# Optimization experiments

Hardware: AMD Instinct MI355X
Metric: run time of the kernel (lower is better)

## Reference

```python
import jax, jax.numpy as jnp
import numpy as np

B, T = 64, 4096
H, I, F = 256, 7, 5
# MLP pyramid: in=H+F=261 -> 2^8..2^3 -> itera_dim
DIMS = [H + F, 256, 128, 64, 32, 16, 8, I]


def _uniform(key, shape, fan_in):
    s = 1.0 / np.sqrt(fan_in)
    return jax.random.uniform(key, shape, jnp.float32, -s, s)


def setup_inputs() -> dict:
    key = jax.random.key(0)
    ks = jax.random.split(key, 32)
    inp = {"x": jax.random.normal(ks[0], (B, T, I + F), jnp.float32)}
    # RNN params (torch nn.RNN layout: W_ih [H,I], W_hh [H,H])
    inp["W_ih"] = _uniform(ks[1], (H, I), H)
    inp["W_hh"] = _uniform(ks[2], (H, H), H)
    inp["b_ih"] = _uniform(ks[3], (H,), H)
    inp["b_hh"] = _uniform(ks[4], (H,), H)
    # fc_V linears
    for j, (din, dout) in enumerate(zip(DIMS[:-1], DIMS[1:])):
        inp[f"W{j}"] = _uniform(ks[5 + 2 * j], (dout, din), din)
        inp[f"b{j}"] = _uniform(ks[6 + 2 * j], (dout,), din)
    return inp


def reference(x, W_ih, W_hh, b_ih, b_hh,
              W0, b0, W1, b1, W2, b2, W3, b3, W4, b4, W5, b5, W6, b6):
    x_itera = x[..., :I]          # [B,T,I]
    x_fixed = x[..., I:]          # [B,T,F]
    # precompute input projection for the whole sequence (one big GEMM)
    xW = jnp.einsum('bti,hi->bth', x_itera, W_ih) + b_ih + b_hh  # [B,T,H]

    def step(h, xw_t):
        h = jnp.tanh(xw_t + h @ W_hh.T)
        return h, h

    h0 = jnp.zeros((x.shape[0], H), x.dtype)
    h_last, ht = jax.lax.scan(step, h0, jnp.swapaxes(xW, 0, 1))  # ht: [T,B,H]
    ht = jnp.swapaxes(ht, 0, 1)                                  # [B,T,H]

    z = jnp.concatenate([ht, x_fixed], axis=-1)                  # [B,T,H+F]
    for W, b in ((W0, b0), (W1, b1), (W2, b2), (W3, b3), (W4, b4), (W5, b5)):
        z = jax.nn.leaky_relu(z @ W.T + b, 0.01)
    ot = z @ W6.T + b6                                           # [B,T,I]
    return ot, h_last[None]                                      # ht_last: [1,B,H]
```

## Files before the change

kernel.cpp:

```cpp
#include <hip/hip_runtime.h>

#define BB 64
#define TT 4096
#define HH 256
#define NTOK (BB * TT)

typedef _Float16 f16;
typedef _Float16 f16x2 __attribute__((ext_vector_type(2)));
typedef _Float16 f16x8 __attribute__((ext_vector_type(8)));
typedef float f32x4 __attribute__((ext_vector_type(4)));
typedef unsigned int uint;
typedef unsigned short ushort;
typedef uint uint4v __attribute__((ext_vector_type(4)));

__device__ __forceinline__ f16x2 u2h(uint u) { return __builtin_bit_cast(f16x2, u); }

__device__ __forceinline__ float fdot2(f16x2 a, f16x2 b, float c) {
    return __builtin_amdgcn_fdot2(a, b, c, false);
}

__device__ __forceinline__ float dpp_xor1(float v) {
    int t = __builtin_amdgcn_update_dpp(0, __builtin_bit_cast(int, v), 0xB1, 0xF, 0xF, true);
    return __builtin_bit_cast(float, t);
}
__device__ __forceinline__ float dpp_xor2(float v) {
    int t = __builtin_amdgcn_update_dpp(0, __builtin_bit_cast(int, v), 0x4E, 0xF, 0xF, true);
    return __builtin_bit_cast(float, t);
}

__device__ __forceinline__ uint packf16(float a, float b) {
    ushort lo = __builtin_bit_cast(ushort, (f16)a);
    ushort hi = __builtin_bit_cast(ushort, (f16)b);
    return (uint)lo | ((uint)hi << 16);
}

__global__ __launch_bounds__(256) void rnn_wswz_kernel(const float* __restrict__ Whh,
                                                       uint* __restrict__ Wsw) {
    int gid = blockIdx.x * 256 + threadIdx.x;
    if (gid >= 256 * 128) return;
    int tid = gid >> 7, rem = gid & 127;
    int q = rem >> 5, i = rem & 31;
    int qd = tid >> 2, s = tid & 3;
    int row = 4 * qd + (q ^ s);
    int col = 64 * s + 2 * i;
    Wsw[gid] = packf16(Whh[row * 256 + col], Whh[row * 256 + col + 1]);
}

__global__ __launch_bounds__(256) void bfrag_prep_kernel(const float* __restrict__ W,
                                                         uint4v* __restrict__ dst,
                                                         int N, int Kreal, int KS, int NT) {
    int gid = blockIdx.x * 256 + threadIdx.x;
    if (gid >= NT * KS * 64) return;
    int lane = gid & 63;
    int t = gid >> 6;
    int ks = t % KS, nt = t / KS;
    int n = nt * 16 + (lane & 15);
    int kb = ks * 32 + (lane >> 4) * 8;
    float f[8];
#pragma unroll
    for (int j = 0; j < 8; ++j) {
        int k = kb + j;
        f[j] = (n < N && k < Kreal) ? W[n * Kreal + k] : 0.f;
    }
    uint4v v;
    v.x = packf16(f[0], f[1]);
    v.y = packf16(f[2], f[3]);
    v.z = packf16(f[4], f[5]);
    v.w = packf16(f[6], f[7]);
    dst[gid] = v;
}

__global__ __launch_bounds__(256) __attribute__((amdgpu_waves_per_eu(1, 1))) void rnn_kernel(
        const float* __restrict__ x, const uint* __restrict__ Wsw,
        const float* __restrict__ Wih, const float* __restrict__ bih,
        const float* __restrict__ bhh, f16* __restrict__ ht, float* __restrict__ hlast) {
    const int b = blockIdx.x, tid = threadIdx.x;
    const int s = tid & 3;
    __shared__ __align__(16) char hbuf[2][576];
    __shared__ uint4 xs[2][128];

    uint4v wv[32];
    {
        const uint4v* wp = (const uint4v*)(Wsw + (size_t)tid * 128);
#pragma unroll
        for (int i = 0; i < 32; ++i) wv[i] = wp[i];
    }
#pragma unroll
    for (int i = 0; i < 32; ++i) asm volatile("" : "+v"(wv[i]));

    float wih[7];
#pragma unroll
    for (int i = 0; i < 7; ++i) wih[i] = Wih[tid * 7 + i];
    const float bias = bih[tid] + bhh[tid];

    const float* xb = x + (size_t)b * TT * 12;
    uint4 xpre = make_uint4(0, 0, 0, 0);
    if (tid < 128) {
        int row = tid >> 1, u = tid & 1;
        xs[0][row * 2 + u] = *(const uint4*)(xb + row * 12 + u * 4);
        xpre = *(const uint4*)(xb + (64 + row) * 12 + u * 4);
    }
    if (tid < 144) ((uint*)hbuf[0])[tid] = 0;
    __syncthreads();

    f16* htp = ht + (size_t)b * TT * 256 + tid;
    ushort hst[16];

    for (int tb = 0; tb < 256; ++tb) {
#pragma unroll
        for (int k = 0; k < 16; ++k) {
            const int t = tb * 16 + k;
            const int cur = k & 1;
            const int tile = (t >> 6) & 1, tstep = t & 63;

            const float4 xa = ((const float4*)xs[tile])[tstep * 2];
            const float4 xc = ((const float4*)xs[tile])[tstep * 2 + 1];
            float xw = fmaf(xa.x, wih[0], bias);
            xw = fmaf(xa.y, wih[1], xw);
            xw = fmaf(xa.z, wih[2], xw);
            xw = fmaf(xa.w, wih[3], xw);
            xw = fmaf(xc.x, wih[4], xw);
            xw = fmaf(xc.y, wih[5], xw);
            xw = fmaf(xc.z, wih[6], xw);

            const uint4* hq = (const uint4*)(hbuf[cur] + s * 144);
            uint hhv[32];
#pragma unroll
            for (int i = 0; i < 8; ++i) {
                uint4 v = hq[i];
                hhv[4 * i + 0] = v.x;
                hhv[4 * i + 1] = v.y;
                hhv[4 * i + 2] = v.z;
                hhv[4 * i + 3] = v.w;
            }

            float acc[4] = {0.f, 0.f, 0.f, 0.f};
#pragma unroll
            for (int q = 0; q < 4; ++q)
#pragma unroll
                for (int i = 0; i < 8; ++i) {
                    uint4v w = wv[q * 8 + i];
                    acc[q] = fdot2(u2h(hhv[4 * i + 0]), u2h(w.x), acc[q]);
                    acc[q] = fdot2(u2h(hhv[4 * i + 1]), u2h(w.y), acc[q]);
                    acc[q] = fdot2(u2h(hhv[4 * i + 2]), u2h(w.z), acc[q]);
                    acc[q] = fdot2(u2h(hhv[4 * i + 3]), u2h(w.w), acc[q]);
                }

            float uu = acc[0] + dpp_xor1(acc[1]);
            float vv = acc[2] + dpp_xor1(acc[3]);
            float pre = uu + dpp_xor2(vv) + xw;

            float e = __expf(-2.0f * pre);
            float r = __builtin_amdgcn_rcpf(1.0f + e);
            float h = fmaf(2.0f, r, -1.0f);

            f16 hf = (f16)h;
            *(f16*)(hbuf[cur ^ 1] + (tid >> 6) * 144 + (tid & 63) * 2) = hf;
            hst[k] = __builtin_bit_cast(ushort, hf);
            if (k == 15 && tb == 255) hlast[b * 256 + tid] = h;

            if (tstep == 32 && tid < 128) {
                int row = tid >> 1, u = tid & 1;
                xs[tile ^ 1][row * 2 + u] = xpre;
                int nt = (t & ~63) + 128 + row;
                if (nt > TT - 1) nt = TT - 1;
                xpre = *(const uint4*)(xb + nt * 12 + u * 4);
            }
            asm volatile("s_waitcnt lgkmcnt(0)\n\ts_barrier" ::: "memory");
        }
        const size_t base = (size_t)(tb * 16) * 256;
#pragma unroll
        for (int k = 0; k < 16; ++k)
            htp[base + (size_t)k * 256] = __builtin_bit_cast(f16, hst[k]);
    }
}

struct MlpB {
    const uint4v* bf[7];
    const float* bias[7];
};

template <int KS, int NT, bool MSPLIT>
__device__ __forceinline__ void mfma_layer(const uint4v* __restrict__ Bf,
                                           const float* __restrict__ bias, int Nreal,
                                           const uint4v* zin, uint4v* zout,
                                           int w, int lane, int m15, int q) {
    constexpr int NW = MSPLIT ? NT : (NT / 4);
    constexpr int MW = MSPLIT ? 1 : 4;
    const int ntb = MSPLIT ? 0 : w * NW;
    const int mtb = MSPLIT ? w : 0;
    f32x4 acc[MW][NW];
#pragma unroll
    for (int i = 0; i < MW; ++i)
#pragma unroll
        for (int j = 0; j < NW; ++j) acc[i][j] = (f32x4){0.f, 0.f, 0.f, 0.f};

#pragma unroll
    for (int ks = 0; ks < KS; ++ks) {
        f16x8 a[MW];
#pragma unroll
        for (int mt = 0; mt < MW; ++mt)
            a[mt] = __builtin_bit_cast(f16x8, zin[((mtb + mt) * 16 + m15) * 37 + ks * 4 + q]);
#pragma unroll
        for (int nt = 0; nt < NW; ++nt) {
            f16x8 b = __builtin_bit_cast(f16x8, Bf[((size_t)(ntb + nt) * KS + ks) * 64 + lane]);
#pragma unroll
            for (int mt = 0; mt < MW; ++mt)
                acc[mt][nt] =
                    __builtin_amdgcn_mfma_f32_16x16x32_f16(a[mt], b, acc[mt][nt], 0, 0, 0);
        }
    }
    f16* zo = (f16*)zout;
#pragma unroll
    for (int nt = 0; nt < NW; ++nt) {
        const int col = (ntb + nt) * 16 + m15;
        const float bv = (col < Nreal) ? bias[col] : 0.f;
#pragma unroll
        for (int mt = 0; mt < MW; ++mt) {
#pragma unroll
            for (int r = 0; r < 4; ++r) {
                float v = acc[mt][nt][r] + bv;
                v = fmaxf(v, 0.01f * v);
                const int row = (mtb + mt) * 16 + q * 4 + r;
                zo[row * 296 + col] = (f16)v;
            }
        }
    }
}

__global__ __launch_bounds__(256) void mlp_kernel(const f16* __restrict__ ht,
                                                  const float* __restrict__ x,
                                                  MlpB P, float* __restrict__ out) {
    __shared__ uint4v z0[64 * 37];
    __shared__ uint4v z1[64 * 37];
    const int tid = threadIdx.x;
    const int w = tid >> 6, lane = tid & 63;
    const int m15 = lane & 15, q = lane >> 4;
    const int tok0 = blockIdx.x * 64;

    for (int i = tid; i < 64 * 32; i += 256) {
        int r = i >> 5, u = i & 31;
        z0[r * 37 + u] = ((const uint4v*)(ht + (size_t)(tok0 + r) * 256))[u];
    }
    for (int i = tid; i < 64 * 5; i += 256) {
        int r = i / 5, u = 32 + (i % 5);
        uint4v v = {0u, 0u, 0u, 0u};
        if (u == 32) {
            const float* xp = x + (size_t)(tok0 + r) * 12 + 7;
            v.x = packf16(xp[0], xp[1]);
            v.y = packf16(xp[2], xp[3]);
            v.z = packf16(xp[4], 0.f);
        }
        z0[r * 37 + u] = v;
    }
    __syncthreads();

    mfma_layer<9, 16, false>(P.bf[0], P.bias[0], 256, z0, z1, w, lane, m15, q);
    __syncthreads();
    mfma_layer<8, 8, false>(P.bf[1], P.bias[1], 128, z1, z0, w, lane, m15, q);
    __syncthreads();
    mfma_layer<4, 4, false>(P.bf[2], P.bias[2], 64, z0, z1, w, lane, m15, q);
    __syncthreads();
    mfma_layer<2, 2, true>(P.bf[3], P.bias[3], 32, z1, z0, w, lane, m15, q);
    __syncthreads();
    mfma_layer<1, 1, true>(P.bf[4], P.bias[4], 16, z0, z1, w, lane, m15, q);
    __syncthreads();
    mfma_layer<1, 1, true>(P.bf[5], P.bias[5], 8, z1, z0, w, lane, m15, q);
    __syncthreads();

    {
        f16x8 a = __builtin_bit_cast(f16x8, z0[(w * 16 + m15) * 37 + q]);
        f16x8 b = __builtin_bit_cast(f16x8, P.bf[6][lane]);
        f32x4 acc = (f32x4){0.f, 0.f, 0.f, 0.f};
        acc = __builtin_amdgcn_mfma_f32_16x16x32_f16(a, b, acc, 0, 0, 0);
        if (m15 < 7) {
            const float bv = P.bias[6][m15];
#pragma unroll
            for (int r = 0; r < 4; ++r)
                out[(size_t)(tok0 + w * 16 + q * 4 + r) * 7 + m15] = acc[r] + bv;
        }
    }
}

extern "C" void kernel_launch(void* const* d_in, const int* in_sizes, int n_in,
                              void* d_out, int out_size, void* d_ws, size_t ws_size,
                              hipStream_t stream) {
    const float* x = (const float*)d_in[0];
    const float* Wih = (const float*)d_in[1];
    const float* Whh = (const float*)d_in[2];
    const float* bih = (const float*)d_in[3];
    const float* bhh = (const float*)d_in[4];
    const float* W[7];
    const float* bb[7];
    for (int j = 0; j < 7; ++j) {
        W[j] = (const float*)d_in[5 + 2 * j];
        bb[j] = (const float*)d_in[6 + 2 * j];
    }
    float* out = (float*)d_out;

    static const int Kd[7] = {261, 256, 128, 64, 32, 16, 8};
    static const int Nd[7] = {256, 128, 64, 32, 16, 8, 7};
    static const int KSd[7] = {9, 8, 4, 2, 1, 1, 1};
    static const int NTd[7] = {16, 8, 4, 2, 1, 1, 1};

    char* ws = (char*)d_ws;
    f16* ht = (f16*)ws;
    size_t off = (size_t)NTOK * HH * 2;
    uint* Wsw = (uint*)(ws + off);
    off += (size_t)256 * 128 * 4;
    uint4v* bfp[7];
    for (int j = 0; j < 7; ++j) {
        bfp[j] = (uint4v*)(ws + off);
        off += (size_t)NTd[j] * KSd[j] * 64 * 16;
    }

    rnn_wswz_kernel<<<128, 256, 0, stream>>>(Whh, Wsw);
    for (int j = 0; j < 7; ++j) {
        int cnt = NTd[j] * KSd[j] * 64;
        bfrag_prep_kernel<<<(cnt + 255) / 256, 256, 0, stream>>>(W[j], bfp[j], Nd[j], Kd[j],
                                                                 KSd[j], NTd[j]);
    }

    rnn_kernel<<<BB, 256, 0, stream>>>(x, Wsw, Wih, bih, bhh, ht, out + (size_t)NTOK * 7);

    MlpB P;
    for (int j = 0; j < 7; ++j) {
        P.bf[j] = bfp[j];
        P.bias[j] = bb[j];
    }
    mlp_kernel<<<NTOK / 64, 256, 0, stream>>>(ht, x, P, out);
}
```

Before: 1.930 ms.

## Split RNN recurrence across 512 threads with two hidden rows per quad

The recurrent kernel now runs 512 threads per batch block instead of 256. Each thread holds half as many W_hh fragments in registers (16 instead of 32 uint4), and each quad computes two hidden units instead of four, so the reduction needs fewer DPP steps. The goal is to shorten the per-timestep serial dot-product chain and ease register pressure. The cost is twice as many waves joining each barrier and redundant tanh work, since only half the threads write results.

```diff
diff --git a/kernel.cpp b/kernel.cpp
--- a/kernel.cpp
+++ b/kernel.cpp
@@ -37,11 +37,11 @@
 __global__ __launch_bounds__(256) void rnn_wswz_kernel(const float* __restrict__ Whh,
                                                        uint* __restrict__ Wsw) {
     int gid = blockIdx.x * 256 + threadIdx.x;
-    if (gid >= 256 * 128) return;
-    int tid = gid >> 7, rem = gid & 127;
+    if (gid >= 512 * 64) return;
+    int tid = gid >> 6, rem = gid & 63;
     int q = rem >> 5, i = rem & 31;
-    int qd = tid >> 2, s = tid & 3;
-    int row = 4 * qd + (q ^ s);
+    int rd = tid >> 2, s = tid & 3;
+    int row = 2 * rd + (q ^ (s & 1));
     int col = 64 * s + 2 * i;
     Wsw[gid] = packf16(Whh[row * 256 + col], Whh[row * 256 + col + 1]);
 }
@@ -70,28 +70,30 @@
     dst[gid] = v;
 }
 
-__global__ __launch_bounds__(256) __attribute__((amdgpu_waves_per_eu(1, 1))) void rnn_kernel(
+__global__ __launch_bounds__(512) __attribute__((amdgpu_waves_per_eu(2, 2))) void rnn_kernel(
         const float* __restrict__ x, const uint* __restrict__ Wsw,
         const float* __restrict__ Wih, const float* __restrict__ bih,
         const float* __restrict__ bhh, f16* __restrict__ ht, float* __restrict__ hlast) {
     const int b = blockIdx.x, tid = threadIdx.x;
     const int s = tid & 3;
+    const int r = ((tid >> 2) << 1) | (tid & 1);
+    const bool writer = (tid & 2) == 0;
     __shared__ __align__(16) char hbuf[2][576];
     __shared__ uint4 xs[2][128];
 
-    uint4v wv[32];
+    uint4v wv[16];
     {
-        const uint4v* wp = (const uint4v*)(Wsw + (size_t)tid * 128);
-#pragma unroll
-        for (int i = 0; i < 32; ++i) wv[i] = wp[i];
-    }
-#pragma unroll
-    for (int i = 0; i < 32; ++i) asm volatile("" : "+v"(wv[i]));
+        const uint4v* wp = (const uint4v*)(Wsw + (size_t)tid * 64);
+#pragma unroll
+        for (int i = 0; i < 16; ++i) wv[i] = wp[i];
+    }
+#pragma unroll
+    for (int i = 0; i < 16; ++i) asm volatile("" : "+v"(wv[i]));
 
     float wih[7];
 #pragma unroll
-    for (int i = 0; i < 7; ++i) wih[i] = Wih[tid * 7 + i];
-    const float bias = bih[tid] + bhh[tid];
+    for (int i = 0; i < 7; ++i) wih[i] = Wih[r * 7 + i];
+    const float bias = bih[r] + bhh[r];
 
     const float* xb = x + (size_t)b * TT * 12;
     uint4 xpre = make_uint4(0, 0, 0, 0);
@@ -103,7 +105,7 @@
     if (tid < 144) ((uint*)hbuf[0])[tid] = 0;
     __syncthreads();
 
-    f16* htp = ht + (size_t)b * TT * 256 + tid;
+    f16* htp = ht + (size_t)b * TT * 256 + r;
     ushort hst[16];
 
     for (int tb = 0; tb < 256; ++tb) {
@@ -124,40 +126,31 @@
             xw = fmaf(xc.z, wih[6], xw);
 
             const uint4* hq = (const uint4*)(hbuf[cur] + s * 144);
-            uint hhv[32];
+            float acc[2] = {0.f, 0.f};
 #pragma unroll
             for (int i = 0; i < 8; ++i) {
                 uint4 v = hq[i];
-                hhv[4 * i + 0] = v.x;
-                hhv[4 * i + 1] = v.y;
-                hhv[4 * i + 2] = v.z;
-                hhv[4 * i + 3] = v.w;
+#pragma unroll
+                for (int q = 0; q < 2; ++q) {
+                    uint4v w = wv[q * 8 + i];
+                    acc[q] = fdot2(u2h(v.x), u2h(w.x), acc[q]);
+                    acc[q] = fdot2(u2h(v.y), u2h(w.y), acc[q]);
+                    acc[q] = fdot2(u2h(v.z), u2h(w.z), acc[q]);
+                    acc[q] = fdot2(u2h(v.w), u2h(w.w), acc[q]);
+                }
             }
 
-            float acc[4] = {0.f, 0.f, 0.f, 0.f};
-#pragma unroll
-            for (int q = 0; q < 4; ++q)
-#pragma unroll
-                for (int i = 0; i < 8; ++i) {
-                    uint4v w = wv[q * 8 + i];
-                    acc[q] = fdot2(u2h(hhv[4 * i + 0]), u2h(w.x), acc[q]);
-                    acc[q] = fdot2(u2h(hhv[4 * i + 1]), u2h(w.y), acc[q]);
-                    acc[q] = fdot2(u2h(hhv[4 * i + 2]), u2h(w.z), acc[q]);
-                    acc[q] = fdot2(u2h(hhv[4 * i + 3]), u2h(w.w), acc[q]);
-                }
-
             float uu = acc[0] + dpp_xor1(acc[1]);
-            float vv = acc[2] + dpp_xor1(acc[3]);
-            float pre = uu + dpp_xor2(vv) + xw;
+            float pre = uu + dpp_xor2(uu) + xw;
 
             float e = __expf(-2.0f * pre);
-            float r = __builtin_amdgcn_rcpf(1.0f + e);
-            float h = fmaf(2.0f, r, -1.0f);
+            float rr = __builtin_amdgcn_rcpf(1.0f + e);
+            float h = fmaf(2.0f, rr, -1.0f);
 
             f16 hf = (f16)h;
-            *(f16*)(hbuf[cur ^ 1] + (tid >> 6) * 144 + (tid & 63) * 2) = hf;
+            if (writer) *(f16*)(hbuf[cur ^ 1] + (r >> 6) * 144 + (r & 63) * 2) = hf;
             hst[k] = __builtin_bit_cast(ushort, hf);
-            if (k == 15 && tb == 255) hlast[b * 256 + tid] = h;
+            if (k == 15 && tb == 255 && writer) hlast[b * 256 + r] = h;
 
             if (tstep == 32 && tid < 128) {
                 int row = tid >> 1, u = tid & 1;
@@ -168,10 +161,12 @@
             }
             asm volatile("s_waitcnt lgkmcnt(0)\n\ts_barrier" ::: "memory");
         }
-        const size_t base = (size_t)(tb * 16) * 256;
-#pragma unroll
-        for (int k = 0; k < 16; ++k)
-            htp[base + (size_t)k * 256] = __builtin_bit_cast(f16, hst[k]);
+        if (writer) {
+            const size_t base = (size_t)(tb * 16) * 256;
+#pragma unroll
+            for (int k = 0; k < 16; ++k)
+                htp[base + (size_t)k * 256] = __builtin_bit_cast(f16, hst[k]);
+        }
     }
 }
 
@@ -307,7 +302,7 @@
     f16* ht = (f16*)ws;
     size_t off = (size_t)NTOK * HH * 2;
     uint* Wsw = (uint*)(ws + off);
-    off += (size_t)256 * 128 * 4;
+    off += (size_t)512 * 64 * 4;
     uint4v* bfp[7];
     for (int j = 0; j < 7; ++j) {
         bfp[j] = (uint4v*)(ws + off);
@@ -321,7 +316,7 @@
                                                                  KSd[j], NTd[j]);
     }
 
-    rnn_kernel<<<BB, 256, 0, stream>>>(x, Wsw, Wih, bih, bhh, ht, out + (size_t)NTOK * 7);
+    rnn_kernel<<<BB, 512, 0, stream>>>(x, Wsw, Wih, bih, bhh, ht, out + (size_t)NTOK * 7);
 
     MlpB P;
     for (int j = 0; j < 7; ++j) {
```

After: 2.063 ms. 1.07x slower.

## Compute RNN recurrent matvec with MFMA instead of fdot2 reductions

Applied to the files above, without the earlier changes.

Repacks W_hh into MFMA A-fragments and performs the per-step hidden-state matvec with 16x16x32 f16 MFMA, broadcasting h as the B operand and selecting each lane's output from the accumulator. This removes the long fdot2 chains and DPP cross-lane reductions on the sequential critical path. It remaps which hidden unit each thread owns and stores ht every step rather than batching 16 steps, trading redundant MFMA columns and more frequent global stores for shorter dependent latency.

```diff
diff --git a/kernel.cpp b/kernel.cpp
--- a/kernel.cpp
+++ b/kernel.cpp
@@ -13,21 +13,6 @@
 typedef unsigned short ushort;
 typedef uint uint4v __attribute__((ext_vector_type(4)));
 
-__device__ __forceinline__ f16x2 u2h(uint u) { return __builtin_bit_cast(f16x2, u); }
-
-__device__ __forceinline__ float fdot2(f16x2 a, f16x2 b, float c) {
-    return __builtin_amdgcn_fdot2(a, b, c, false);
-}
-
-__device__ __forceinline__ float dpp_xor1(float v) {
-    int t = __builtin_amdgcn_update_dpp(0, __builtin_bit_cast(int, v), 0xB1, 0xF, 0xF, true);
-    return __builtin_bit_cast(float, t);
-}
-__device__ __forceinline__ float dpp_xor2(float v) {
-    int t = __builtin_amdgcn_update_dpp(0, __builtin_bit_cast(int, v), 0x4E, 0xF, 0xF, true);
-    return __builtin_bit_cast(float, t);
-}
-
 __device__ __forceinline__ uint packf16(float a, float b) {
     ushort lo = __builtin_bit_cast(ushort, (f16)a);
     ushort hi = __builtin_bit_cast(ushort, (f16)b);
@@ -35,15 +20,21 @@
 }
 
 __global__ __launch_bounds__(256) void rnn_wswz_kernel(const float* __restrict__ Whh,
-                                                       uint* __restrict__ Wsw) {
+                                                       uint4v* __restrict__ Wsw) {
     int gid = blockIdx.x * 256 + threadIdx.x;
-    if (gid >= 256 * 128) return;
-    int tid = gid >> 7, rem = gid & 127;
-    int q = rem >> 5, i = rem & 31;
-    int qd = tid >> 2, s = tid & 3;
-    int row = 4 * qd + (q ^ s);
-    int col = 64 * s + 2 * i;
-    Wsw[gid] = packf16(Whh[row * 256 + col], Whh[row * 256 + col + 1]);
+    if (gid >= 8192) return;
+    int tid = gid >> 5, fi = gid & 31;
+    int mt = fi >> 3, ks = fi & 7;
+    int lane = tid & 63, w = tid >> 6;
+    int hd = w * 64 + mt * 16 + (lane & 15);
+    int kb = ks * 32 + ((lane >> 4) << 3);
+    const float* p = Whh + hd * 256 + kb;
+    uint4v v;
+    v.x = packf16(p[0], p[1]);
+    v.y = packf16(p[2], p[3]);
+    v.z = packf16(p[4], p[5]);
+    v.w = packf16(p[6], p[7]);
+    Wsw[gid] = v;
 }
 
 __global__ __launch_bounds__(256) void bfrag_prep_kernel(const float* __restrict__ W,
@@ -71,17 +62,19 @@
 }
 
 __global__ __launch_bounds__(256) __attribute__((amdgpu_waves_per_eu(1, 1))) void rnn_kernel(
-        const float* __restrict__ x, const uint* __restrict__ Wsw,
+        const float* __restrict__ x, const uint4v* __restrict__ Wsw,
         const float* __restrict__ Wih, const float* __restrict__ bih,
         const float* __restrict__ bhh, f16* __restrict__ ht, float* __restrict__ hlast) {
     const int b = blockIdx.x, tid = threadIdx.x;
-    const int s = tid & 3;
-    __shared__ __align__(16) char hbuf[2][576];
+    const int lane = tid & 63, w = tid >> 6;
+    const int q = lane >> 4, bl = lane & 15;
+    const int d = w * 64 + ((bl >> 2) << 4) + (q << 2) + (bl & 3);
+    __shared__ __align__(16) f16 hbuf[2][256];
     __shared__ uint4 xs[2][128];
 
     uint4v wv[32];
     {
-        const uint4v* wp = (const uint4v*)(Wsw + (size_t)tid * 128);
+        const uint4v* wp = Wsw + (size_t)tid * 32;
 #pragma unroll
         for (int i = 0; i < 32; ++i) wv[i] = wp[i];
     }
@@ -90,8 +83,8 @@
 
     float wih[7];
 #pragma unroll
-    for (int i = 0; i < 7; ++i) wih[i] = Wih[tid * 7 + i];
-    const float bias = bih[tid] + bhh[tid];
+    for (int i = 0; i < 7; ++i) wih[i] = Wih[d * 7 + i];
+    const float bias = bih[d] + bhh[d];
 
     const float* xb = x + (size_t)b * TT * 12;
     uint4 xpre = make_uint4(0, 0, 0, 0);
@@ -99,12 +92,11 @@
         int row = tid >> 1, u = tid & 1;
         xs[0][row * 2 + u] = *(const uint4*)(xb + row * 12 + u * 4);
         xpre = *(const uint4*)(xb + (64 + row) * 12 + u * 4);
-    }
-    if (tid < 144) ((uint*)hbuf[0])[tid] = 0;
-    __syncthreads();
-
-    f16* htp = ht + (size_t)b * TT * 256 + tid;
-    ushort hst[16];
+        ((uint*)hbuf[0])[tid] = 0;
+    }
+    __syncthreads();
+
+    f16* htp = ht + (size_t)b * TT * 256 + d;
 
     for (int tb = 0; tb < 256; ++tb) {
 #pragma unroll
@@ -123,41 +115,42 @@
             xw = fmaf(xc.y, wih[5], xw);
             xw = fmaf(xc.z, wih[6], xw);
 
-            const uint4* hq = (const uint4*)(hbuf[cur] + s * 144);
-            uint hhv[32];
-#pragma unroll
-            for (int i = 0; i < 8; ++i) {
-                uint4 v = hq[i];
-                hhv[4 * i + 0] = v.x;
-                hhv[4 * i + 1] = v.y;
-                hhv[4 * i + 2] = v.z;
-                hhv[4 * i + 3] = v.w;
+            const uint4v* hq = (const uint4v*)hbuf[cur];
+            uint4v hfr[8];
+#pragma unroll
+            for (int ks = 0; ks < 8; ++ks) hfr[ks] = hq[ks * 4 + q];
+
+            f32x4 acc[4];
+#pragma unroll
+            for (int mt = 0; mt < 4; ++mt) acc[mt] = (f32x4){0.f, 0.f, 0.f, 0.f};
+#pragma unroll
+            for (int ks = 0; ks < 8; ++ks) {
+                f16x8 hb = __builtin_bit_cast(f16x8, hfr[ks]);
+#pragma unroll
+                for (int mt = 0; mt < 4; ++mt)
+                    acc[mt] = __builtin_amdgcn_mfma_f32_16x16x32_f16(
+                        __builtin_bit_cast(f16x8, wv[mt * 8 + ks]), hb, acc[mt], 0, 0, 0);
             }
 
-            float acc[4] = {0.f, 0.f, 0.f, 0.f};
-#pragma unroll
-            for (int q = 0; q < 4; ++q)
-#pragma unroll
-                for (int i = 0; i < 8; ++i) {
-                    uint4v w = wv[q * 8 + i];
-                    acc[q] = fdot2(u2h(hhv[4 * i + 0]), u2h(w.x), acc[q]);
-                    acc[q] = fdot2(u2h(hhv[4 * i + 1]), u2h(w.y), acc[q]);
-                    acc[q] = fdot2(u2h(hhv[4 * i + 2]), u2h(w.z), acc[q]);
-                    acc[q] = fdot2(u2h(hhv[4 * i + 3]), u2h(w.w), acc[q]);
-                }
-
-            float uu = acc[0] + dpp_xor1(acc[1]);
-            float vv = acc[2] + dpp_xor1(acc[3]);
-            float pre = uu + dpp_xor2(vv) + xw;
+            float t0[4];
+#pragma unroll
+            for (int mt = 0; mt < 4; ++mt) {
+                float a01 = (bl & 1) ? acc[mt][1] : acc[mt][0];
+                float a23 = (bl & 1) ? acc[mt][3] : acc[mt][2];
+                t0[mt] = (bl & 2) ? a23 : a01;
+            }
+            float u0 = (bl & 4) ? t0[1] : t0[0];
+            float u1 = (bl & 4) ? t0[3] : t0[2];
+            float pre = ((bl & 8) ? u1 : u0) + xw;
 
             float e = __expf(-2.0f * pre);
-            float r = __builtin_amdgcn_rcpf(1.0f + e);
-            float h = fmaf(2.0f, r, -1.0f);
+            float rr = __builtin_amdgcn_rcpf(1.0f + e);
+            float h = fmaf(2.0f, rr, -1.0f);
 
             f16 hf = (f16)h;
-            *(f16*)(hbuf[cur ^ 1] + (tid >> 6) * 144 + (tid & 63) * 2) = hf;
-            hst[k] = __builtin_bit_cast(ushort, hf);
-            if (k == 15 && tb == 255) hlast[b * 256 + tid] = h;
+            hbuf[cur ^ 1][d] = hf;
+            htp[(size_t)t * 256] = hf;
+            if (tb == 255 && k == 15) hlast[b * 256 + d] = h;
 
             if (tstep == 32 && tid < 128) {
                 int row = tid >> 1, u = tid & 1;
@@ -168,10 +161,6 @@
             }
             asm volatile("s_waitcnt lgkmcnt(0)\n\ts_barrier" ::: "memory");
         }
-        const size_t base = (size_t)(tb * 16) * 256;
-#pragma unroll
-        for (int k = 0; k < 16; ++k)
-            htp[base + (size_t)k * 256] = __builtin_bit_cast(f16, hst[k]);
     }
 }
 
@@ -306,15 +295,15 @@
     char* ws = (char*)d_ws;
     f16* ht = (f16*)ws;
     size_t off = (size_t)NTOK * HH * 2;
-    uint* Wsw = (uint*)(ws + off);
-    off += (size_t)256 * 128 * 4;
+    uint4v* Wsw = (uint4v*)(ws + off);
+    off += (size_t)8192 * 16;
     uint4v* bfp[7];
     for (int j = 0; j < 7; ++j) {
         bfp[j] = (uint4v*)(ws + off);
         off += (size_t)NTd[j] * KSd[j] * 64 * 16;
     }
 
-    rnn_wswz_kernel<<<128, 256, 0, stream>>>(Whh, Wsw);
+    rnn_wswz_kernel<<<32, 256, 0, stream>>>(Whh, Wsw);
     for (int j = 0; j < 7; ++j) {
         int cnt = NTd[j] * KSd[j] * 64;
         bfrag_prep_kernel<<<(cnt + 255) / 256, 256, 0, stream>>>(W[j], bfp[j], Nd[j], Kd[j],
```

Measured after the change: 2.112 ms. 1.09x slower.
